# Kernel optimization log

Hardware: AMD Instinct MI355X
Metric: run time of the kernel (lower is better)

## Reference

```python
import jax, jax.numpy as jnp
import numpy as np

B, N, H, E, D = 8, 2048, 1024, 8, 2048


def setup_inputs() -> dict:
    key = jax.random.key(0)
    k = jax.random.split(key, 5)
    x = jax.random.normal(k[0], (B, N, H), dtype=jnp.float32)
    Wr = jax.random.normal(k[1], (H, E), dtype=jnp.float32) * 0.02
    br = jnp.zeros((E,), dtype=jnp.float32)
    W1 = jax.random.normal(k[2], (E, H, D), dtype=jnp.float32) * 0.02
    b1 = jnp.zeros((E, D), dtype=jnp.float32)
    W2 = jax.random.normal(k[3], (E, D, H), dtype=jnp.float32) * 0.02
    b2 = jnp.zeros((E, H), dtype=jnp.float32)
    return {"x": x, "Wr": Wr, "br": br, "W1": W1, "b1": b1, "W2": W2, "b2": b2}


def reference(x, Wr, br, W1, b1, W2, b2):
    # x: [B,N,H]; router v1, top-1, eval mode (no expert dropout)
    Bx, Nx, Hx = x.shape
    Ex = Wr.shape[1]
    x_flat = x.reshape(Bx * Nx, Hx)                      # [T,H]
    logits = x_flat @ Wr + br                            # [T,E]
    probs = jax.nn.softmax(logits, axis=-1)              # [T,E]
    expert_idx = jnp.argmax(probs, axis=-1)              # [T]

    out_flat = jnp.zeros_like(x_flat)
    for e in range(Ex):  # small fixed loop over experts
        h = jax.nn.gelu(x_flat @ W1[e] + b1[e], approximate=False)  # exact erf GELU (torch default)
        eout = h @ W2[e] + b2[e]                         # [T,H]
        out_flat = jnp.where((expert_idx == e)[:, None], eout, out_flat)

    out = x + out_flat.reshape(Bx, Nx, Hx)               # residual

    p_i = probs.mean(axis=0)                             # [E]
    balance_loss = Ex * jnp.sum(p_i ** 2)
    EPS = 1e-8
    entropy = -jnp.sum(probs * jnp.log(probs + EPS), axis=-1)
    entropy_loss = entropy.mean()
    tokens_per_expert = jnp.bincount(expert_idx, length=Ex)
    return out, balance_loss, entropy_loss, tokens_per_expert
```

## Files before the change

kernel.cpp:

```cpp
#include <hip/hip_runtime.h>
#include <math.h>

#define TT 16384
#define HH 1024
#define DD 2048
#define EE 8
#define MAXTILES 160

typedef float f32x4 __attribute__((ext_vector_type(4)));
typedef __bf16 bf16x8 __attribute__((ext_vector_type(8)));

__device__ __forceinline__ unsigned short f2bf(float f) {
  union { float f; unsigned u; } v; v.f = f;
  unsigned r = v.u + 0x7FFFu + ((v.u >> 16) & 1u);
  return (unsigned short)(r >> 16);
}

__device__ __forceinline__ void gl2lds16(const unsigned short* g, unsigned short* l) {
  __builtin_amdgcn_global_load_lds(
      (const __attribute__((address_space(1))) void*)g,
      (__attribute__((address_space(3))) void*)l, 16, 0, 0);
}

__global__ void k_init(int* counts, float* probs_sum, float* ent_sum) {
  int t = threadIdx.x;
  if (t < EE) { counts[t] = 0; probs_sum[t] = 0.f; }
  if (t == 0) *ent_sum = 0.f;
}

__global__ __launch_bounds__(256) void k_transpose(const float* __restrict__ src,
                                                   unsigned short* __restrict__ dst,
                                                   int R, int C) {
  __shared__ float tile[32][33];
  int tilesC = C / 32, tilesR = R / 32;
  int bid = blockIdx.x;
  int e = bid / (tilesR * tilesC);
  int rem = bid % (tilesR * tilesC);
  int tr = rem / tilesC, tc = rem % tilesC;
  const float* s = src + (size_t)e * R * C;
  unsigned short* d = dst + (size_t)e * R * C;
  int tx = threadIdx.x & 31, ty = threadIdx.x >> 5;
#pragma unroll
  for (int i = 0; i < 4; ++i)
    tile[ty + i * 8][tx] = s[(size_t)(tr * 32 + ty + i * 8) * C + tc * 32 + tx];
  __syncthreads();
#pragma unroll
  for (int i = 0; i < 4; ++i) {
    int rr = ty + i * 8;
    d[(size_t)(tc * 32 + rr) * R + tr * 32 + tx] = f2bf(tile[tx][rr]);
  }
}

__global__ __launch_bounds__(256) void k_router(const float* __restrict__ x,
                                                const float* __restrict__ Wr,
                                                const float* __restrict__ br,
                                                int* __restrict__ eidx,
                                                float* __restrict__ probs_sum,
                                                float* __restrict__ ent_sum,
                                                int* __restrict__ counts,
                                                unsigned short* __restrict__ xb) {
  __shared__ float s_p[EE];
  __shared__ int   s_c[EE];
  __shared__ float s_e;
  int tid = threadIdx.x;
  if (tid < EE) { s_p[tid] = 0.f; s_c[tid] = 0; }
  if (tid == 0) s_e = 0.f;
  __syncthreads();
  int lane = tid & 63, w = tid >> 6;
  for (int tt = 0; tt < 4; ++tt) {
    int token = blockIdx.x * 16 + w * 4 + tt;
    double acc[EE];
#pragma unroll
    for (int e = 0; e < EE; ++e) acc[e] = 0.0;
    const float* xr = x + (size_t)token * HH;
    unsigned short* xo = xb + (size_t)token * HH;
    for (int i = 0; i < 16; ++i) {
      int hh = i * 64 + lane;
      float xf = xr[hh];
      xo[hh] = f2bf(xf);
      double xv = (double)xf;
      const float* wr = Wr + (size_t)hh * EE;
#pragma unroll
      for (int e = 0; e < EE; ++e) acc[e] += xv * (double)wr[e];
    }
#pragma unroll
    for (int off = 32; off > 0; off >>= 1) {
#pragma unroll
      for (int e = 0; e < EE; ++e) acc[e] += __shfl_down(acc[e], off);
    }
    if (lane == 0) {
      double l[EE];
#pragma unroll
      for (int e = 0; e < EE; ++e) l[e] = acc[e] + (double)br[e];
      double m = l[0]; int am = 0;
#pragma unroll
      for (int e = 1; e < EE; ++e) { if (l[e] > m) { m = l[e]; am = e; } }
      double p[EE]; double s = 0.0;
#pragma unroll
      for (int e = 0; e < EE; ++e) { p[e] = exp(l[e] - m); s += p[e]; }
      double inv = 1.0 / s; double ent = 0.0;
#pragma unroll
      for (int e = 0; e < EE; ++e) { p[e] *= inv; ent -= p[e] * log(p[e] + 1e-8); }
      eidx[token] = am;
#pragma unroll
      for (int e = 0; e < EE; ++e) atomicAdd(&s_p[e], (float)p[e]);
      atomicAdd(&s_e, (float)ent);
      atomicAdd(&s_c[am], 1);
    }
  }
  __syncthreads();
  if (tid < EE) { atomicAdd(&probs_sum[tid], s_p[tid]); atomicAdd(&counts[tid], s_c[tid]); }
  if (tid == 0) atomicAdd(ent_sum, s_e);
}

__global__ void k_scan(const int* counts, const float* probs_sum, const float* ent_sum,
                       int* offsets, int* cursor,
                       int* tileE, int* tileR0, int* tileEnd, int* nTiles,
                       float* out_scalars) {
  if (threadIdx.x != 0) return;
  int off = 0, nt = 0;
  for (int e = 0; e < EE; ++e) {
    offsets[e] = off; cursor[e] = off;
    int c = counts[e];
    for (int r = 0; r < c; r += 128) {
      tileE[nt] = e; tileR0[nt] = off + r; tileEnd[nt] = off + c; ++nt;
    }
    off += c;
  }
  offsets[EE] = off;
  *nTiles = nt;
  float bal = 0.f;
  for (int e = 0; e < EE; ++e) { float pi = probs_sum[e] / (float)TT; bal += pi * pi; }
  out_scalars[0] = (float)EE * bal;
  out_scalars[1] = *ent_sum / (float)TT;
  for (int e = 0; e < EE; ++e) out_scalars[2 + e] = (float)counts[e];
}

__global__ __launch_bounds__(256) void k_perm(const int* __restrict__ eidx,
                                              int* cursor, int* __restrict__ perm) {
  int t = blockIdx.x * 256 + threadIdx.x;
  int lane = threadIdx.x & 63;
  int mye = eidx[t];
  int pos = 0;
#pragma unroll
  for (int e = 0; e < EE; ++e) {
    unsigned long long mask = __ballot(mye == e);
    if (mask == 0ull) continue;
    int leader = __ffsll(mask) - 1;
    int base = 0;
    if (lane == leader) base = atomicAdd(&cursor[e], __popcll(mask));
    base = __shfl(base, leader);
    if (mye == e) pos = base + (int)__popcll(mask & ((1ull << lane) - 1ull));
  }
  perm[pos] = t;
}


__global__ __launch_bounds__(256) void k_gemm1(const unsigned short* __restrict__ xb,
                                               const unsigned short* __restrict__ Wt1,
                                               const float* __restrict__ b1,
                                               const int* __restrict__ perm,
                                               const int* __restrict__ tileE,
                                               const int* __restrict__ tileR0,
                                               const int* __restrict__ tileEnd,
                                               const int* __restrict__ nTiles,
                                               unsigned short* __restrict__ hbuf) {
  int tile = blockIdx.y;
  if (tile >= *nTiles) return;
  int e = tileE[tile], r0 = tileR0[tile], rend = tileEnd[tile];
  int c0 = blockIdx.x * 128;
  __shared__ __align__(16) unsigned short As[128 * 32];
  __shared__ __align__(16) unsigned short Bs[128 * 32];
  int tid = threadIdx.x, lane = tid & 63, w = tid >> 6;
  int wr = w >> 1, wc = w & 1;
  int quad = lane >> 4, l16 = lane & 15;
  int srow = lane >> 2, seg = lane & 3;
  int ar0 = w * 32 + srow, ar1 = ar0 + 16;
  int g0 = r0 + ar0; if (g0 >= rend) g0 = rend - 1;
  int g1 = r0 + ar1; if (g1 >= rend) g1 = rend - 1;
  const unsigned short* aG0 = xb + (size_t)perm[g0] * HH + seg * 8;
  const unsigned short* aG1 = xb + (size_t)perm[g1] * HH + seg * 8;
  const unsigned short* bBase = Wt1 + (size_t)e * ((size_t)DD * HH);
  const unsigned short* bG0 = bBase + (size_t)(c0 + ar0) * HH + seg * 8;
  const unsigned short* bG1 = bBase + (size_t)(c0 + ar1) * HH + seg * 8;
  unsigned short* aL0 = &As[(w * 32 + 0) * 32];
  unsigned short* aL1 = &As[(w * 32 + 16) * 32];
  unsigned short* bL0 = &Bs[(w * 32 + 0) * 32];
  unsigned short* bL1 = &Bs[(w * 32 + 16) * 32];
  f32x4 acc[4][4] = {};
  for (int k0 = 0; k0 < HH; k0 += 32) {
    gl2lds16(aG0 + k0, aL0);
    gl2lds16(aG1 + k0, aL1);
    gl2lds16(bG0 + k0, bL0);
    gl2lds16(bG1 + k0, bL1);
    __syncthreads();
    bf16x8 a[4], b[4];
#pragma unroll
    for (int i = 0; i < 4; ++i)
      a[i] = *(const bf16x8*)&As[(wr * 64 + i * 16 + l16) * 32 + quad * 8];
#pragma unroll
    for (int j = 0; j < 4; ++j)
      b[j] = *(const bf16x8*)&Bs[(wc * 64 + j * 16 + l16) * 32 + quad * 8];
#pragma unroll
    for (int i = 0; i < 4; ++i)
#pragma unroll
      for (int j = 0; j < 4; ++j)
        acc[i][j] = __builtin_amdgcn_mfma_f32_16x16x32_bf16(a[i], b[j], acc[i][j], 0, 0, 0);
    __syncthreads();
  }
  float bias[4];
#pragma unroll
  for (int j = 0; j < 4; ++j) bias[j] = b1[e * DD + c0 + wc * 64 + j * 16 + l16];
#pragma unroll
  for (int i = 0; i < 4; ++i) {
#pragma unroll
    for (int r = 0; r < 4; ++r) {
      int gr = r0 + wr * 64 + i * 16 + quad * 4 + r;
      if (gr < rend) {
#pragma unroll
        for (int j = 0; j < 4; ++j) {
          int col = c0 + wc * 64 + j * 16 + l16;
          float v = acc[i][j][r] + bias[j];
          v = 0.5f * v * (1.0f + erff(v * 0.70710678118654752f));
          hbuf[(size_t)gr * DD + col] = f2bf(v);
        }
      }
    }
  }
}

__global__ __launch_bounds__(256) void k_gemm2(const unsigned short* __restrict__ hbuf,
                                               const unsigned short* __restrict__ Wt2,
                                               const float* __restrict__ b2,
                                               const float* __restrict__ x,
                                               const int* __restrict__ perm,
                                               const int* __restrict__ tileE,
                                               const int* __restrict__ tileR0,
                                               const int* __restrict__ tileEnd,
                                               const int* __restrict__ nTiles,
                                               float* __restrict__ outp) {
  int tile = blockIdx.y;
  if (tile >= *nTiles) return;
  int e = tileE[tile], r0 = tileR0[tile], rend = tileEnd[tile];
  int c0 = blockIdx.x * 128;
  __shared__ __align__(16) unsigned short As[128 * 32];
  __shared__ __align__(16) unsigned short Bs[128 * 32];
  int tid = threadIdx.x, lane = tid & 63, w = tid >> 6;
  int wr = w >> 1, wc = w & 1;
  int quad = lane >> 4, l16 = lane & 15;
  int srow = lane >> 2, seg = lane & 3;
  int ar0 = w * 32 + srow, ar1 = ar0 + 16;
  int g0 = r0 + ar0; if (g0 >= rend) g0 = rend - 1;
  int g1 = r0 + ar1; if (g1 >= rend) g1 = rend - 1;
  const unsigned short* aG0 = hbuf + (size_t)g0 * DD + seg * 8;
  const unsigned short* aG1 = hbuf + (size_t)g1 * DD + seg * 8;
  const unsigned short* bBase = Wt2 + (size_t)e * ((size_t)HH * DD);
  const unsigned short* bG0 = bBase + (size_t)(c0 + ar0) * DD + seg * 8;
  const unsigned short* bG1 = bBase + (size_t)(c0 + ar1) * DD + seg * 8;
  unsigned short* aL0 = &As[(w * 32 + 0) * 32];
  unsigned short* aL1 = &As[(w * 32 + 16) * 32];
  unsigned short* bL0 = &Bs[(w * 32 + 0) * 32];
  unsigned short* bL1 = &Bs[(w * 32 + 16) * 32];
  f32x4 acc[4][4] = {};
  for (int k0 = 0; k0 < DD; k0 += 32) {
    gl2lds16(aG0 + k0, aL0);
    gl2lds16(aG1 + k0, aL1);
    gl2lds16(bG0 + k0, bL0);
    gl2lds16(bG1 + k0, bL1);
    __syncthreads();
    bf16x8 a[4], b[4];
#pragma unroll
    for (int i = 0; i < 4; ++i)
      a[i] = *(const bf16x8*)&As[(wr * 64 + i * 16 + l16) * 32 + quad * 8];
#pragma unroll
    for (int j = 0; j < 4; ++j)
      b[j] = *(const bf16x8*)&Bs[(wc * 64 + j * 16 + l16) * 32 + quad * 8];
#pragma unroll
    for (int i = 0; i < 4; ++i)
#pragma unroll
      for (int j = 0; j < 4; ++j)
        acc[i][j] = __builtin_amdgcn_mfma_f32_16x16x32_bf16(a[i], b[j], acc[i][j], 0, 0, 0);
    __syncthreads();
  }
  float bias[4];
#pragma unroll
  for (int j = 0; j < 4; ++j) bias[j] = b2[e * HH + c0 + wc * 64 + j * 16 + l16];
#pragma unroll
  for (int i = 0; i < 4; ++i) {
#pragma unroll
    for (int r = 0; r < 4; ++r) {
      int gr = r0 + wr * 64 + i * 16 + quad * 4 + r;
      if (gr < rend) {
        int tok = perm[gr];
#pragma unroll
        for (int j = 0; j < 4; ++j) {
          int col = c0 + wc * 64 + j * 16 + l16;
          size_t oi = (size_t)tok * HH + col;
          outp[oi] = x[oi] + bias[j] + acc[i][j][r];
        }
      }
    }
  }
}

extern "C" void kernel_launch(void* const* d_in, const int* in_sizes, int n_in,
                              void* d_out, int out_size, void* d_ws, size_t ws_size,
                              hipStream_t stream) {
  const float* x  = (const float*)d_in[0];
  const float* Wr = (const float*)d_in[1];
  const float* br = (const float*)d_in[2];
  const float* W1 = (const float*)d_in[3];
  const float* b1 = (const float*)d_in[4];
  const float* W2 = (const float*)d_in[5];
  const float* b2 = (const float*)d_in[6];
  float* outp = (float*)d_out;

  char* ws = (char*)d_ws;
  int*   counts    = (int*)(ws + 0);
  int*   cursor    = (int*)(ws + 64);
  int*   nTiles    = (int*)(ws + 128);
  float* probs_sum = (float*)(ws + 192);
  float* ent_sum   = (float*)(ws + 256);
  int*   offsets   = (int*)(ws + 320);
  int*   tileE     = (int*)(ws + 512);
  int*   tileR0    = (int*)(ws + 2048);
  int*   tileEnd   = (int*)(ws + 3584);
  int*   eidx      = (int*)(ws + 8192);
  int*   perm      = (int*)(ws + 8192 + 4 * (size_t)TT);
  size_t off = 8192 + 8 * (size_t)TT;
  unsigned short* xb   = (unsigned short*)(ws + off); off += (size_t)TT * HH * 2;
  unsigned short* Wt1  = (unsigned short*)(ws + off); off += (size_t)EE * DD * HH * 2;
  unsigned short* Wt2  = (unsigned short*)(ws + off); off += (size_t)EE * HH * DD * 2;
  unsigned short* hbuf = (unsigned short*)(ws + off); off += (size_t)TT * DD * 2;

  k_init<<<1, 64, 0, stream>>>(counts, probs_sum, ent_sum);
  k_transpose<<<EE * (HH / 32) * (DD / 32), 256, 0, stream>>>(W1, Wt1, HH, DD);
  k_transpose<<<EE * (DD / 32) * (HH / 32), 256, 0, stream>>>(W2, Wt2, DD, HH);
  k_router<<<TT / 16, 256, 0, stream>>>(x, Wr, br, eidx, probs_sum, ent_sum, counts, xb);
  k_scan<<<1, 64, 0, stream>>>(counts, probs_sum, ent_sum, offsets, cursor,
                               tileE, tileR0, tileEnd, nTiles, outp + (size_t)TT * HH);
  k_perm<<<TT / 256, 256, 0, stream>>>(eidx, cursor, perm);
  dim3 g1(DD / 128, MAXTILES);
  k_gemm1<<<g1, 256, 0, stream>>>(xb, Wt1, b1, perm, tileE, tileR0, tileEnd, nTiles, hbuf);
  dim3 g2(HH / 128, MAXTILES);
  k_gemm2<<<g2, 256, 0, stream>>>(hbuf, Wt2, b2, x, perm, tileE, tileR0, tileEnd, nTiles, outp);
}
```

Baseline: 598.3 us.

## Double K-tile to 64 with XOR-swizzled LDS and swap grid axes in MoE GEMMs

Both expert GEMM kernels now stage a 64-wide K slice per iteration instead of 32, which halves the number of barrier pairs per K loop. LDS rows are stored with an XOR swizzle on the 16-byte column chunk so the MFMA fragment reads avoid bank conflicts. The grid is transposed so consecutive blocks walk token tiles, with the column block on the y axis, which changes which blocks share weight and activation data in cache. LDS per block doubles, which may lower occupancy.

```diff
diff --git a/kernel.cpp b/kernel.cpp
--- a/kernel.cpp
+++ b/kernel.cpp
@@ -6,6 +6,7 @@
 #define DD 2048
 #define EE 8
 #define MAXTILES 160
+#define BK 64
 
 typedef float f32x4 __attribute__((ext_vector_type(4)));
 typedef __bf16 bf16x8 __attribute__((ext_vector_type(8)));
@@ -165,47 +166,53 @@
                                                const int* __restrict__ tileEnd,
                                                const int* __restrict__ nTiles,
                                                unsigned short* __restrict__ hbuf) {
-  int tile = blockIdx.y;
+  int tile = blockIdx.x;
   if (tile >= *nTiles) return;
   int e = tileE[tile], r0 = tileR0[tile], rend = tileEnd[tile];
-  int c0 = blockIdx.x * 128;
-  __shared__ __align__(16) unsigned short As[128 * 32];
-  __shared__ __align__(16) unsigned short Bs[128 * 32];
+  int c0 = blockIdx.y * 128;
+  __shared__ __align__(16) unsigned short As[128 * BK];
+  __shared__ __align__(16) unsigned short Bs[128 * BK];
   int tid = threadIdx.x, lane = tid & 63, w = tid >> 6;
   int wr = w >> 1, wc = w & 1;
   int quad = lane >> 4, l16 = lane & 15;
-  int srow = lane >> 2, seg = lane & 3;
-  int ar0 = w * 32 + srow, ar1 = ar0 + 16;
-  int g0 = r0 + ar0; if (g0 >= rend) g0 = rend - 1;
-  int g1 = r0 + ar1; if (g1 >= rend) g1 = rend - 1;
-  const unsigned short* aG0 = xb + (size_t)perm[g0] * HH + seg * 8;
-  const unsigned short* aG1 = xb + (size_t)perm[g1] * HH + seg * 8;
+  int cpos = lane & 7, rsub = lane >> 3;
+  int cg8 = ((cpos ^ rsub) * 8);
+  const unsigned short* aG[4]; const unsigned short* bG[4];
+  unsigned short* aL[4]; unsigned short* bL[4];
   const unsigned short* bBase = Wt1 + (size_t)e * ((size_t)DD * HH);
-  const unsigned short* bG0 = bBase + (size_t)(c0 + ar0) * HH + seg * 8;
-  const unsigned short* bG1 = bBase + (size_t)(c0 + ar1) * HH + seg * 8;
-  unsigned short* aL0 = &As[(w * 32 + 0) * 32];
-  unsigned short* aL1 = &As[(w * 32 + 16) * 32];
-  unsigned short* bL0 = &Bs[(w * 32 + 0) * 32];
-  unsigned short* bL1 = &Bs[(w * 32 + 16) * 32];
+#pragma unroll
+  for (int i = 0; i < 4; ++i) {
+    int ar = w * 32 + i * 8 + rsub;
+    int g = r0 + ar; if (g >= rend) g = rend - 1;
+    aG[i] = xb + (size_t)perm[g] * HH + cg8;
+    bG[i] = bBase + (size_t)(c0 + ar) * HH + cg8;
+    aL[i] = As + (w * 4 + i) * 512;
+    bL[i] = Bs + (w * 4 + i) * 512;
+  }
   f32x4 acc[4][4] = {};
-  for (int k0 = 0; k0 < HH; k0 += 32) {
-    gl2lds16(aG0 + k0, aL0);
-    gl2lds16(aG1 + k0, aL1);
-    gl2lds16(bG0 + k0, bL0);
-    gl2lds16(bG1 + k0, bL1);
+  int swz = (l16 & 7);
+  for (int k0 = 0; k0 < HH; k0 += BK) {
+#pragma unroll
+    for (int i = 0; i < 4; ++i) gl2lds16(aG[i] + k0, aL[i]);
+#pragma unroll
+    for (int i = 0; i < 4; ++i) gl2lds16(bG[i] + k0, bL[i]);
     __syncthreads();
-    bf16x8 a[4], b[4];
-#pragma unroll
-    for (int i = 0; i < 4; ++i)
-      a[i] = *(const bf16x8*)&As[(wr * 64 + i * 16 + l16) * 32 + quad * 8];
-#pragma unroll
-    for (int j = 0; j < 4; ++j)
-      b[j] = *(const bf16x8*)&Bs[(wc * 64 + j * 16 + l16) * 32 + quad * 8];
-#pragma unroll
-    for (int i = 0; i < 4; ++i)
+#pragma unroll
+    for (int h = 0; h < 2; ++h) {
+      int co = ((h * 4 + quad) ^ swz) * 8;
+      bf16x8 a[4], b[4];
+#pragma unroll
+      for (int i = 0; i < 4; ++i)
+        a[i] = *(const bf16x8*)&As[(wr * 64 + i * 16 + l16) * BK + co];
 #pragma unroll
       for (int j = 0; j < 4; ++j)
-        acc[i][j] = __builtin_amdgcn_mfma_f32_16x16x32_bf16(a[i], b[j], acc[i][j], 0, 0, 0);
+        b[j] = *(const bf16x8*)&Bs[(wc * 64 + j * 16 + l16) * BK + co];
+#pragma unroll
+      for (int i = 0; i < 4; ++i)
+#pragma unroll
+        for (int j = 0; j < 4; ++j)
+          acc[i][j] = __builtin_amdgcn_mfma_f32_16x16x32_bf16(a[i], b[j], acc[i][j], 0, 0, 0);
+    }
     __syncthreads();
   }
   float bias[4];
@@ -239,47 +246,53 @@
                                                const int* __restrict__ tileEnd,
                                                const int* __restrict__ nTiles,
                                                float* __restrict__ outp) {
-  int tile = blockIdx.y;
+  int tile = blockIdx.x;
   if (tile >= *nTiles) return;
   int e = tileE[tile], r0 = tileR0[tile], rend = tileEnd[tile];
-  int c0 = blockIdx.x * 128;
-  __shared__ __align__(16) unsigned short As[128 * 32];
-  __shared__ __align__(16) unsigned short Bs[128 * 32];
+  int c0 = blockIdx.y * 128;
+  __shared__ __align__(16) unsigned short As[128 * BK];
+  __shared__ __align__(16) unsigned short Bs[128 * BK];
   int tid = threadIdx.x, lane = tid & 63, w = tid >> 6;
   int wr = w >> 1, wc = w & 1;
   int quad = lane >> 4, l16 = lane & 15;
-  int srow = lane >> 2, seg = lane & 3;
-  int ar0 = w * 32 + srow, ar1 = ar0 + 16;
-  int g0 = r0 + ar0; if (g0 >= rend) g0 = rend - 1;
-  int g1 = r0 + ar1; if (g1 >= rend) g1 = rend - 1;
-  const unsigned short* aG0 = hbuf + (size_t)g0 * DD + seg * 8;
-  const unsigned short* aG1 = hbuf + (size_t)g1 * DD + seg * 8;
+  int cpos = lane & 7, rsub = lane >> 3;
+  int cg8 = ((cpos ^ rsub) * 8);
+  const unsigned short* aG[4]; const unsigned short* bG[4];
+  unsigned short* aL[4]; unsigned short* bL[4];
   const unsigned short* bBase = Wt2 + (size_t)e * ((size_t)HH * DD);
-  const unsigned short* bG0 = bBase + (size_t)(c0 + ar0) * DD + seg * 8;
-  const unsigned short* bG1 = bBase + (size_t)(c0 + ar1) * DD + seg * 8;
-  unsigned short* aL0 = &As[(w * 32 + 0) * 32];
-  unsigned short* aL1 = &As[(w * 32 + 16) * 32];
-  unsigned short* bL0 = &Bs[(w * 32 + 0) * 32];
-  unsigned short* bL1 = &Bs[(w * 32 + 16) * 32];
+#pragma unroll
+  for (int i = 0; i < 4; ++i) {
+    int ar = w * 32 + i * 8 + rsub;
+    int g = r0 + ar; if (g >= rend) g = rend - 1;
+    aG[i] = hbuf + (size_t)g * DD + cg8;
+    bG[i] = bBase + (size_t)(c0 + ar) * DD + cg8;
+    aL[i] = As + (w * 4 + i) * 512;
+    bL[i] = Bs + (w * 4 + i) * 512;
+  }
   f32x4 acc[4][4] = {};
-  for (int k0 = 0; k0 < DD; k0 += 32) {
-    gl2lds16(aG0 + k0, aL0);
-    gl2lds16(aG1 + k0, aL1);
-    gl2lds16(bG0 + k0, bL0);
-    gl2lds16(bG1 + k0, bL1);
+  int swz = (l16 & 7);
+  for (int k0 = 0; k0 < DD; k0 += BK) {
+#pragma unroll
+    for (int i = 0; i < 4; ++i) gl2lds16(aG[i] + k0, aL[i]);
+#pragma unroll
+    for (int i = 0; i < 4; ++i) gl2lds16(bG[i] + k0, bL[i]);
     __syncthreads();
-    bf16x8 a[4], b[4];
-#pragma unroll
-    for (int i = 0; i < 4; ++i)
-      a[i] = *(const bf16x8*)&As[(wr * 64 + i * 16 + l16) * 32 + quad * 8];
-#pragma unroll
-    for (int j = 0; j < 4; ++j)
-      b[j] = *(const bf16x8*)&Bs[(wc * 64 + j * 16 + l16) * 32 + quad * 8];
-#pragma unroll
-    for (int i = 0; i < 4; ++i)
+#pragma unroll
+    for (int h = 0; h < 2; ++h) {
+      int co = ((h * 4 + quad) ^ swz) * 8;
+      bf16x8 a[4], b[4];
+#pragma unroll
+      for (int i = 0; i < 4; ++i)
+        a[i] = *(const bf16x8*)&As[(wr * 64 + i * 16 + l16) * BK + co];
 #pragma unroll
       for (int j = 0; j < 4; ++j)
-        acc[i][j] = __builtin_amdgcn_mfma_f32_16x16x32_bf16(a[i], b[j], acc[i][j], 0, 0, 0);
+        b[j] = *(const bf16x8*)&Bs[(wc * 64 + j * 16 + l16) * BK + co];
+#pragma unroll
+      for (int i = 0; i < 4; ++i)
+#pragma unroll
+        for (int j = 0; j < 4; ++j)
+          acc[i][j] = __builtin_amdgcn_mfma_f32_16x16x32_bf16(a[i], b[j], acc[i][j], 0, 0, 0);
+    }
     __syncthreads();
   }
   float bias[4];
@@ -340,8 +353,8 @@
   k_scan<<<1, 64, 0, stream>>>(counts, probs_sum, ent_sum, offsets, cursor,
                                tileE, tileR0, tileEnd, nTiles, outp + (size_t)TT * HH);
   k_perm<<<TT / 256, 256, 0, stream>>>(eidx, cursor, perm);
-  dim3 g1(DD / 128, MAXTILES);
+  dim3 g1(MAXTILES, DD / 128);
   k_gemm1<<<g1, 256, 0, stream>>>(xb, Wt1, b1, perm, tileE, tileR0, tileEnd, nTiles, hbuf);
-  dim3 g2(HH / 128, MAXTILES);
+  dim3 g2(MAXTILES, HH / 128);
   k_gemm2<<<g2, 256, 0, stream>>>(hbuf, Wt2, b2, x, perm, tileE, tileR0, tileEnd, nTiles, outp);
 }
```

New measurement: 629.0 us. 1.05x slower.
